# Kernel optimization log

Measured on AMD Instinct MI355X. Metric: run time of the kernel, lower is better.

## Reference

```python
import jax, jax.numpy as jnp
import numpy as np

GROUP = 64  # group_size from module


def setup_inputs() -> dict:
    key = jax.random.key(0)
    ks = jax.random.split(key, 7)
    B, S, N, K = 4, 2048, 4096, 4096  # in_features=N, out_features=K
    G = N // GROUP
    x = jax.random.normal(ks[0], (B, S, N), dtype=jnp.float32)
    W_q = jax.random.randint(ks[1], (K, N), 0, 16, dtype=jnp.int32)  # 4-bit codes
    scales = jax.random.uniform(ks[2], (K, G), dtype=jnp.float32, minval=0.01, maxval=1.0)
    zeros = jax.random.uniform(ks[3], (K, G), dtype=jnp.float32, minval=0.0, maxval=15.0)
    mask = jax.random.randint(ks[4], (K, N), 0, 2, dtype=jnp.int32)  # unstructured sparsity mask
    scale2 = jax.random.uniform(ks[5], (K, 1), dtype=jnp.float32, minval=0.5, maxval=1.5)
    bias = jax.random.normal(ks[6], (K,), dtype=jnp.float32)
    return {"x": x, "W_q": W_q, "scales": scales, "zeros": zeros,
            "mask": mask, "scale2": scale2, "bias": bias}


def _dequantize_sparse_sinq(W_q, scales, zeros, mask, scale2, dtype):
    # W_q: (K, N) int codes; scales/zeros: (K, N//GROUP) per-(row,group);
    # scale2: (K, 1) second (Sinkhorn) row scale; mask: (K, N) sparsity mask.
    K, N = W_q.shape
    G = N // GROUP
    Wg = W_q.astype(dtype).reshape(K, G, GROUP)
    W = (Wg - zeros[:, :, None]) * scales[:, :, None]  # grouped affine dequant
    W = W.reshape(K, N) * scale2                       # dual-scale compensation
    W = W * mask.astype(dtype)                         # apply unstructured sparsity
    return W


def reference(x, W_q, scales, zeros, mask, scale2, bias):
    W = _dequantize_sparse_sinq(W_q, scales, zeros, mask, scale2, x.dtype)  # (K, N)
    out = jnp.einsum('bsn,kn->bsk', x, W) + bias  # x @ W.T + bias
    return out
```

## Files before the change

kernel.cpp:

```cpp
#include <hip/hip_runtime.h>


#define M_DIM 8192
#define N_DIM 4096
#define K_DIM 4096
#define BK 32
#define NT (N_DIM / BK)

typedef __bf16 bf16;
typedef __attribute__((ext_vector_type(8))) bf16 bf16x8;
typedef __attribute__((ext_vector_type(4))) float f32x4;

__global__ __launch_bounds__(256) void cvt_x_kernel(const float* __restrict__ x,
                                                    bf16* __restrict__ xb) {
  const long total = (long)M_DIM * N_DIM / 8;
  const long stride = (long)gridDim.x * blockDim.x;
  for (long t = (long)blockIdx.x * blockDim.x + threadIdx.x; t < total; t += stride) {
    const long e = t * 8;
    const float4 v0 = *reinterpret_cast<const float4*>(x + e);
    const float4 v1 = *reinterpret_cast<const float4*>(x + e + 4);
    bf16x8 o;
    o[0] = (bf16)v0.x; o[1] = (bf16)v0.y; o[2] = (bf16)v0.z; o[3] = (bf16)v0.w;
    o[4] = (bf16)v1.x; o[5] = (bf16)v1.y; o[6] = (bf16)v1.z; o[7] = (bf16)v1.w;
    *reinterpret_cast<bf16x8*>(xb + e) = o;
  }
}

__global__ __launch_bounds__(256) void deq_w_kernel(const int* __restrict__ Wq,
                                                    const float* __restrict__ scales,
                                                    const float* __restrict__ zeros,
                                                    const int* __restrict__ mask,
                                                    const float* __restrict__ scale2,
                                                    bf16* __restrict__ wb) {
  const int total = K_DIM * (N_DIM / 8);
  const int stride = gridDim.x * blockDim.x;
  for (int t = blockIdx.x * blockDim.x + threadIdx.x; t < total; t += stride) {
    const int k = t >> 9;
    const int n0 = (t & 511) << 3;
    const int g = n0 >> 6;
    const float s = scales[(k << 6) + g] * scale2[k];
    const float z = zeros[(k << 6) + g];
    const long base = (long)k * N_DIM + n0;
    const int4 q0 = *reinterpret_cast<const int4*>(Wq + base);
    const int4 q1 = *reinterpret_cast<const int4*>(Wq + base + 4);
    const int4 m0 = *reinterpret_cast<const int4*>(mask + base);
    const int4 m1 = *reinterpret_cast<const int4*>(mask + base + 4);
    bf16x8 o;
    o[0] = (bf16)(((float)q0.x - z) * s * (float)m0.x);
    o[1] = (bf16)(((float)q0.y - z) * s * (float)m0.y);
    o[2] = (bf16)(((float)q0.z - z) * s * (float)m0.z);
    o[3] = (bf16)(((float)q0.w - z) * s * (float)m0.w);
    o[4] = (bf16)(((float)q1.x - z) * s * (float)m1.x);
    o[5] = (bf16)(((float)q1.y - z) * s * (float)m1.y);
    o[6] = (bf16)(((float)q1.z - z) * s * (float)m1.z);
    o[7] = (bf16)(((float)q1.w - z) * s * (float)m1.w);
    *reinterpret_cast<bf16x8*>(wb + base) = o;
  }
}

__device__ inline void gload16(const bf16* g, bf16* l) {
  __builtin_amdgcn_global_load_lds(
      (const __attribute__((address_space(1))) void*)g,
      (__attribute__((address_space(3))) void*)l, 16, 0, 0);
}

__global__ __launch_bounds__(512, 2) void gemm_kernel(const bf16* __restrict__ xb,
                                                      const bf16* __restrict__ wb,
                                                      const float* __restrict__ bias,
                                                      float* __restrict__ out) {
  __shared__ bf16 lds[65536];

  const int tid = threadIdx.x;
  const int lane = tid & 63;
  const int w = tid >> 6;
  const int wr = w >> 2;
  const int wc = w & 3;

  const int gid = blockIdx.x;
  const int swz = ((gid & 7) << 6) | (gid >> 3);
  const int bm = swz & 31;
  const int bk = swz >> 5;
  const long m0 = (long)bm * 256;
  const long k0 = (long)bk * 256;

  const bf16* srcA0; const bf16* srcA1; const bf16* srcB0; const bf16* srcB1;
  {
    const int p0 = w * 1024 + lane * 16;
    const int rp0 = p0 >> 7;
    const int v0 = ((p0 >> 4) & 7) ^ (rp0 & 7);
    const int row0 = rp0 * 2 + (v0 >> 2), col0 = (v0 & 3) * 8;
    const int p1 = 8192 + w * 1024 + lane * 16;
    const int rp1 = p1 >> 7;
    const int v1 = ((p1 >> 4) & 7) ^ (rp1 & 7);
    const int row1 = rp1 * 2 + (v1 >> 2), col1 = (v1 & 3) * 8;
    srcA0 = xb + (m0 + row0) * N_DIM + col0;
    srcA1 = xb + (m0 + row1) * N_DIM + col1;
    srcB0 = wb + (k0 + row0) * N_DIM + col0;
    srcB1 = wb + (k0 + row1) * N_DIM + col1;
  }

  const int halfrow = (lane & 15) >> 1;
  const int xsw = (((lane & 1) << 2) | (lane >> 4)) ^ halfrow;
  const int frBase = halfrow * 64 + xsw * 8;
  const int aOff = wr * 4096 + frBase;
  const int bOff = 8192 + wc * 2048 + frBase;

  auto STAGE = [&](int t) {
    bf16* base = lds + (t & 3) * 16384;
    const int ko = t * BK;
    gload16(srcA0 + ko, base + w * 512);
    gload16(srcA1 + ko, base + 4096 + w * 512);
    gload16(srcB0 + ko, base + 8192 + w * 512);
    gload16(srcB1 + ko, base + 12288 + w * 512);
  };

  f32x4 acc[8][4] = {};

  STAGE(0); STAGE(1); STAGE(2);
  asm volatile("s_waitcnt vmcnt(8)" ::: "memory");
  asm volatile("s_barrier" ::: "memory");

  for (int t = 0; t < NT; ++t) {
    const bf16* base = lds + (t & 3) * 16384;
    bf16x8 af[8], bfr[4];
#pragma unroll
    for (int mi = 0; mi < 8; ++mi)
      af[mi] = *reinterpret_cast<const bf16x8*>(base + aOff + mi * 512);
#pragma unroll
    for (int ni = 0; ni < 4; ++ni)
      bfr[ni] = *reinterpret_cast<const bf16x8*>(base + bOff + ni * 512);

    if (t + 3 < NT) STAGE(t + 3);

    if (t < NT - 3)       asm volatile("s_waitcnt vmcnt(8)" ::: "memory");
    else if (t == NT - 3) asm volatile("s_waitcnt vmcnt(4)" ::: "memory");
    else                  asm volatile("s_waitcnt vmcnt(0)" ::: "memory");
    asm volatile("s_waitcnt lgkmcnt(0)" ::: "memory");
    asm volatile("s_barrier" ::: "memory");
    __builtin_amdgcn_sched_barrier(0);

    __builtin_amdgcn_s_setprio(1);
#pragma unroll
    for (int mi = 0; mi < 8; ++mi)
#pragma unroll
      for (int ni = 0; ni < 4; ++ni)
        acc[mi][ni] = __builtin_amdgcn_mfma_f32_16x16x32_bf16(af[mi], bfr[ni],
                                                              acc[mi][ni], 0, 0, 0);
    __builtin_amdgcn_s_setprio(0);
  }

  const int ocol0 = (int)k0 + wc * 64 + (lane & 15);
  const int orow0 = (int)m0 + wr * 128 + (lane >> 4) * 4;
#pragma unroll
  for (int ni = 0; ni < 4; ++ni) {
    const float bv = bias[ocol0 + ni * 16];
#pragma unroll
    for (int mi = 0; mi < 8; ++mi)
#pragma unroll
      for (int r = 0; r < 4; ++r)
        out[(long)(orow0 + mi * 16 + r) * K_DIM + ocol0 + ni * 16] =
            acc[mi][ni][r] + bv;
  }
}

extern "C" void kernel_launch(void* const* d_in, const int* in_sizes, int n_in,
                              void* d_out, int out_size, void* d_ws, size_t ws_size,
                              hipStream_t stream) {
  const float* x      = (const float*)d_in[0];
  const int*   Wq     = (const int*)d_in[1];
  const float* scales = (const float*)d_in[2];
  const float* zeros  = (const float*)d_in[3];
  const int*   mask   = (const int*)d_in[4];
  const float* scale2 = (const float*)d_in[5];
  const float* bias   = (const float*)d_in[6];
  float* out = (float*)d_out;

  bf16* xb = (bf16*)d_ws;
  bf16* wb = (bf16*)((char*)d_ws + (size_t)M_DIM * N_DIM * 2);

  cvt_x_kernel<<<2048, 256, 0, stream>>>(x, xb);
  deq_w_kernel<<<2048, 256, 0, stream>>>(Wq, scales, zeros, mask, scale2, wb);

  gemm_kernel<<<512, 512, 0, stream>>>(xb, wb, bias, out);
}
```

Baseline: 321.3 us.

## Restructure GEMM main loop into ping-pong half-tile stages with interleaved loads

The GEMM main loop moves from a 4-deep ring of BK=32 stages to two 64-wide K buffers. Each 64-wide tile is split into four half-tile phases: LDS fragment reads and global-to-LDS staging of A or B halves are interleaved with 8x2 MFMA blocks, separated by barriers. The goal is to spread memory traffic across the compute and shrink fragment register pressure (the B fragments are split into halves). In exchange it adds many more barriers per K step and a shallower prefetch distance, and the waitcnt bookkeeping is intricate.

```diff
diff --git a/kernel.cpp b/kernel.cpp
--- a/kernel.cpp
+++ b/kernel.cpp
@@ -4,8 +4,7 @@
 #define M_DIM 8192
 #define N_DIM 4096
 #define K_DIM 4096
-#define BK 32
-#define NT (N_DIM / BK)
+#define NTILE 64
 
 typedef __bf16 bf16;
 typedef __attribute__((ext_vector_type(8))) bf16 bf16x8;
@@ -64,6 +63,12 @@
       (__attribute__((address_space(3))) void*)l, 16, 0, 0);
 }
 
+#define BARRIER asm volatile("s_barrier" ::: "memory")
+#define LGKM0   asm volatile("s_waitcnt lgkmcnt(0)" ::: "memory")
+#define VM4     asm volatile("s_waitcnt vmcnt(4)" ::: "memory")
+#define VM0     asm volatile("s_waitcnt vmcnt(0)" ::: "memory")
+#define SBAR    __builtin_amdgcn_sched_barrier(0)
+
 __global__ __launch_bounds__(512, 2) void gemm_kernel(const bf16* __restrict__ xb,
                                                       const bf16* __restrict__ wb,
                                                       const float* __restrict__ bias,
@@ -83,7 +88,7 @@
   const long m0 = (long)bm * 256;
   const long k0 = (long)bk * 256;
 
-  const bf16* srcA0; const bf16* srcA1; const bf16* srcB0; const bf16* srcB1;
+  const bf16 *srcA0, *srcA1, *srcB0, *srcB1;
   {
     const int p0 = w * 1024 + lane * 16;
     const int rp0 = p0 >> 7;
@@ -101,52 +106,92 @@
 
   const int halfrow = (lane & 15) >> 1;
   const int xsw = (((lane & 1) << 2) | (lane >> 4)) ^ halfrow;
-  const int frBase = halfrow * 64 + xsw * 8;
-  const int aOff = wr * 4096 + frBase;
-  const int bOff = 8192 + wc * 2048 + frBase;
-
-  auto STAGE = [&](int t) {
-    bf16* base = lds + (t & 3) * 16384;
-    const int ko = t * BK;
-    gload16(srcA0 + ko, base + w * 512);
-    gload16(srcA1 + ko, base + 4096 + w * 512);
-    gload16(srcB0 + ko, base + 8192 + w * 512);
-    gload16(srcB1 + ko, base + 12288 + w * 512);
-  };
+  const int aBase = wr * 4096 + halfrow * 64 + xsw * 8;
+  const int bBase = wc * 2048 + halfrow * 64 + xsw * 8;
 
   f32x4 acc[8][4] = {};
-
-  STAGE(0); STAGE(1); STAGE(2);
-  asm volatile("s_waitcnt vmcnt(8)" ::: "memory");
-  asm volatile("s_barrier" ::: "memory");
-
-  for (int t = 0; t < NT; ++t) {
-    const bf16* base = lds + (t & 3) * 16384;
-    bf16x8 af[8], bfr[4];
+  bf16x8 a[8], b01[2], b23[2];
+
+  auto LD_A = [&](int bufbase, int kk) {
 #pragma unroll
     for (int mi = 0; mi < 8; ++mi)
-      af[mi] = *reinterpret_cast<const bf16x8*>(base + aOff + mi * 512);
-#pragma unroll
-    for (int ni = 0; ni < 4; ++ni)
-      bfr[ni] = *reinterpret_cast<const bf16x8*>(base + bOff + ni * 512);
-
-    if (t + 3 < NT) STAGE(t + 3);
-
-    if (t < NT - 3)       asm volatile("s_waitcnt vmcnt(8)" ::: "memory");
-    else if (t == NT - 3) asm volatile("s_waitcnt vmcnt(4)" ::: "memory");
-    else                  asm volatile("s_waitcnt vmcnt(0)" ::: "memory");
-    asm volatile("s_waitcnt lgkmcnt(0)" ::: "memory");
-    asm volatile("s_barrier" ::: "memory");
-    __builtin_amdgcn_sched_barrier(0);
-
+      a[mi] = *reinterpret_cast<const bf16x8*>(lds + bufbase + kk * 8192 + aBase + mi * 512);
+  };
+  auto LD_B = [&](bf16x8* b, int bufbase, int kk, int nh) {
+#pragma unroll
+    for (int j = 0; j < 2; ++j)
+      b[j] = *reinterpret_cast<const bf16x8*>(lds + bufbase + 16384 + kk * 8192 + bBase + (nh * 2 + j) * 512);
+  };
+  auto MFMA8x2 = [&](bf16x8* b, int nh) {
     __builtin_amdgcn_s_setprio(1);
 #pragma unroll
     for (int mi = 0; mi < 8; ++mi)
 #pragma unroll
-      for (int ni = 0; ni < 4; ++ni)
-        acc[mi][ni] = __builtin_amdgcn_mfma_f32_16x16x32_bf16(af[mi], bfr[ni],
-                                                              acc[mi][ni], 0, 0, 0);
+      for (int j = 0; j < 2; ++j)
+        acc[mi][nh * 2 + j] = __builtin_amdgcn_mfma_f32_16x16x32_bf16(
+            a[mi], b[j], acc[mi][nh * 2 + j], 0, 0, 0);
     __builtin_amdgcn_s_setprio(0);
+  };
+  auto STAGE2 = [&](const bf16* s0, const bf16* s1, int dstoff) {
+    gload16(s0, lds + dstoff + w * 512);
+    gload16(s1, lds + dstoff + 4096 + w * 512);
+  };
+
+  STAGE2(srcA0, srcA1, 0);
+  STAGE2(srcB0, srcB1, 16384);
+  STAGE2(srcA0 + 32, srcA1 + 32, 8192);
+  STAGE2(srcB0 + 32, srcB1 + 32, 24576);
+  VM4;
+  BARRIER;
+
+  for (int tp = 0; tp < NTILE / 2; ++tp) {
+    const int koA = (2 * tp + 1) * 64;
+    const int koB = (2 * tp + 2) * 64;
+    const bool st = (tp < NTILE / 2 - 1);
+
+    LD_A(0, 0); LD_B(b01, 0, 0, 0);
+    STAGE2(srcA0 + koA, srcA1 + koA, 32768 + 0);
+    BARRIER; LGKM0; SBAR;
+    MFMA8x2(b01, 0); SBAR;
+    BARRIER;
+    LD_B(b23, 0, 0, 1);
+    STAGE2(srcB0 + koA, srcB1 + koA, 32768 + 16384);
+    VM4; BARRIER; LGKM0; SBAR;
+    MFMA8x2(b23, 1); SBAR;
+    BARRIER;
+    LD_A(0, 1); LD_B(b01, 0, 1, 0);
+    STAGE2(srcA0 + koA + 32, srcA1 + koA + 32, 32768 + 8192);
+    BARRIER; LGKM0; SBAR;
+    MFMA8x2(b01, 0); SBAR;
+    BARRIER;
+    LD_B(b23, 0, 1, 1);
+    STAGE2(srcB0 + koA + 32, srcB1 + koA + 32, 32768 + 24576);
+    VM4; BARRIER; LGKM0; SBAR;
+    MFMA8x2(b23, 1); SBAR;
+    BARRIER;
+
+    LD_A(32768, 0); LD_B(b01, 32768, 0, 0);
+    if (st) STAGE2(srcA0 + koB, srcA1 + koB, 0);
+    BARRIER; LGKM0; SBAR;
+    MFMA8x2(b01, 0); SBAR;
+    BARRIER;
+    LD_B(b23, 32768, 0, 1);
+    if (st) STAGE2(srcB0 + koB, srcB1 + koB, 16384);
+    if (st) { VM4; } else { VM0; }
+    BARRIER; LGKM0; SBAR;
+    MFMA8x2(b23, 1); SBAR;
+    BARRIER;
+    LD_A(32768, 1); LD_B(b01, 32768, 1, 0);
+    if (st) STAGE2(srcA0 + koB + 32, srcA1 + koB + 32, 8192);
+    BARRIER; LGKM0; SBAR;
+    MFMA8x2(b01, 0); SBAR;
+    BARRIER;
+    LD_B(b23, 32768, 1, 1);
+    if (st) STAGE2(srcB0 + koB + 32, srcB1 + koB + 32, 24576);
+    if (st) { VM4; } else { VM0; }
+    BARRIER; LGKM0; SBAR;
+    MFMA8x2(b23, 1); SBAR;
+    BARRIER;
   }
 
   const int ocol0 = (int)k0 + wc * 64 + (lane & 15);
```

After: 328.7 us. +2.3%, slower.

## Restructure GEMM mainloop into 64-wide K tiles with quadrant-interleaved loads and MFMAs

Applied to the files above, without the earlier changes.

Raises the K tile from 32 to 64 and replaces the 4-stage ring of small tiles with a double-buffered 64-wide tile. Each tile is split into four MFMA quadrants, with LDS fragment reads and global-to-LDS loads for later tiles issued between them. The aim is to hide global and LDS latency behind MFMA work and to cut barriers and waits per unit of compute. In exchange it adds more barriers inside each tile, and the prefetch/vmcnt bookkeeping is more complex and easier to get wrong.

```diff
diff --git a/kernel.cpp b/kernel.cpp
--- a/kernel.cpp
+++ b/kernel.cpp
@@ -4,8 +4,7 @@
 #define M_DIM 8192
 #define N_DIM 4096
 #define K_DIM 4096
-#define BK 32
-#define NT (N_DIM / BK)
+#define NT 64
 
 typedef __bf16 bf16;
 typedef __attribute__((ext_vector_type(8))) bf16 bf16x8;
@@ -64,6 +63,12 @@
       (__attribute__((address_space(3))) void*)l, 16, 0, 0);
 }
 
+#define BARRIER asm volatile("s_barrier" ::: "memory")
+#define LGKM0   asm volatile("s_waitcnt lgkmcnt(0)" ::: "memory")
+#define VM6     asm volatile("s_waitcnt vmcnt(6)" ::: "memory")
+#define VM0     asm volatile("s_waitcnt vmcnt(0)" ::: "memory")
+#define SBAR    __builtin_amdgcn_sched_barrier(0)
+
 __global__ __launch_bounds__(512, 2) void gemm_kernel(const bf16* __restrict__ xb,
                                                       const bf16* __restrict__ wb,
                                                       const float* __restrict__ bias,
@@ -83,73 +88,100 @@
   const long m0 = (long)bm * 256;
   const long k0 = (long)bk * 256;
 
-  const bf16* srcA0; const bf16* srcA1; const bf16* srcB0; const bf16* srcB1;
-  {
-    const int p0 = w * 1024 + lane * 16;
-    const int rp0 = p0 >> 7;
-    const int v0 = ((p0 >> 4) & 7) ^ (rp0 & 7);
-    const int row0 = rp0 * 2 + (v0 >> 2), col0 = (v0 & 3) * 8;
-    const int p1 = 8192 + w * 1024 + lane * 16;
-    const int rp1 = p1 >> 7;
-    const int v1 = ((p1 >> 4) & 7) ^ (rp1 & 7);
-    const int row1 = rp1 * 2 + (v1 >> 2), col1 = (v1 & 3) * 8;
-    srcA0 = xb + (m0 + row0) * N_DIM + col0;
-    srcA1 = xb + (m0 + row1) * N_DIM + col1;
-    srcB0 = wb + (k0 + row0) * N_DIM + col0;
-    srcB1 = wb + (k0 + row1) * N_DIM + col1;
-  }
-
-  const int halfrow = (lane & 15) >> 1;
-  const int xsw = (((lane & 1) << 2) | (lane >> 4)) ^ halfrow;
-  const int frBase = halfrow * 64 + xsw * 8;
-  const int aOff = wr * 4096 + frBase;
-  const int bOff = 8192 + wc * 2048 + frBase;
-
-  auto STAGE = [&](int t) {
-    bf16* base = lds + (t & 3) * 16384;
-    const int ko = t * BK;
-    gload16(srcA0 + ko, base + w * 512);
-    gload16(srcA1 + ko, base + 4096 + w * 512);
-    gload16(srcB0 + ko, base + 8192 + w * 512);
-    gload16(srcB1 + ko, base + 12288 + w * 512);
-  };
+  const int browA = tid >> 3;
+  const int slotA = (tid & 7) ^ (browA & 7);
+  const bf16* baseA = xb + (m0 + browA) * N_DIM + slotA * 8;
+  const int u = tid & 255;
+  const int wcb = tid >> 8;
+  const int browB = u >> 3;
+  const int slotB = (u & 7) ^ (browB & 7);
+  const bf16* baseB = wb + (k0 + wcb * 64 + browB) * N_DIM + slotB * 8;
+
+  const int ln15 = lane & 15;
+  const int x0 = (lane >> 4) ^ (lane & 7);
+  int aoffk[2], boffk[2];
+#pragma unroll
+  for (int kk = 0; kk < 2; ++kk) {
+    const int x = x0 ^ (kk << 2);
+    aoffk[kk] = (wr * 128 + ln15) * 64 + x * 8;
+    boffk[kk] = 16384 + (wc * 64 + ln15) * 64 + x * 8;
+  }
 
   f32x4 acc[8][4] = {};
-
-  STAGE(0); STAGE(1); STAGE(2);
-  asm volatile("s_waitcnt vmcnt(8)" ::: "memory");
-  asm volatile("s_barrier" ::: "memory");
-
-  for (int t = 0; t < NT; ++t) {
-    const bf16* base = lds + (t & 3) * 16384;
-    bf16x8 af[8], bfr[4];
-#pragma unroll
-    for (int mi = 0; mi < 8; ++mi)
-      af[mi] = *reinterpret_cast<const bf16x8*>(base + aOff + mi * 512);
-#pragma unroll
-    for (int ni = 0; ni < 4; ++ni)
-      bfr[ni] = *reinterpret_cast<const bf16x8*>(base + bOff + ni * 512);
-
-    if (t + 3 < NT) STAGE(t + 3);
-
-    if (t < NT - 3)       asm volatile("s_waitcnt vmcnt(8)" ::: "memory");
-    else if (t == NT - 3) asm volatile("s_waitcnt vmcnt(4)" ::: "memory");
-    else                  asm volatile("s_waitcnt vmcnt(0)" ::: "memory");
-    asm volatile("s_waitcnt lgkmcnt(0)" ::: "memory");
-    asm volatile("s_barrier" ::: "memory");
-    __builtin_amdgcn_sched_barrier(0);
-
+  bf16x8 af[4][2], bfA[2][2], bfB[2][2];
+
+  auto STA = [&](int tt, int bsel, int h) {
+    const bf16* s = baseA + (long)(h * 64) * N_DIM + tt * 64;
+    bf16* d = lds + bsel * 32768 + h * 4096 + (tid << 3);
+    gload16(s, d);
+    gload16(s + (long)128 * N_DIM, d + 8192);
+  };
+  auto STB = [&](int tt, int bsel, int h) {
+    const bf16* s = baseB + (long)(h * 32) * N_DIM + tt * 64;
+    bf16* d = lds + bsel * 32768 + 16384 + wcb * 4096 + h * 2048 + (u << 3);
+    gload16(s, d);
+    gload16(s + (long)128 * N_DIM, d + 8192);
+  };
+  auto LDA = [&](int cb, int mh) {
+#pragma unroll
+    for (int mf = 0; mf < 4; ++mf)
+#pragma unroll
+      for (int kk = 0; kk < 2; ++kk)
+        af[mf][kk] = *reinterpret_cast<const bf16x8*>(
+            lds + cb + aoffk[kk] + mh * 4096 + mf * 1024);
+  };
+  auto LDB = [&](bf16x8 (*bf)[2], int cb, int nh) {
+#pragma unroll
+    for (int nf = 0; nf < 2; ++nf)
+#pragma unroll
+      for (int kk = 0; kk < 2; ++kk)
+        bf[nf][kk] = *reinterpret_cast<const bf16x8*>(
+            lds + cb + boffk[kk] + nh * 2048 + nf * 1024);
+  };
+  auto MFMA_Q = [&](bf16x8 (*bf)[2], int mh, int nh) {
     __builtin_amdgcn_s_setprio(1);
 #pragma unroll
-    for (int mi = 0; mi < 8; ++mi)
-#pragma unroll
-      for (int ni = 0; ni < 4; ++ni)
-        acc[mi][ni] = __builtin_amdgcn_mfma_f32_16x16x32_bf16(af[mi], bfr[ni],
-                                                              acc[mi][ni], 0, 0, 0);
+    for (int kk = 0; kk < 2; ++kk)
+#pragma unroll
+      for (int mf = 0; mf < 4; ++mf)
+#pragma unroll
+        for (int nf = 0; nf < 2; ++nf)
+          acc[mh * 4 + mf][nh * 2 + nf] = __builtin_amdgcn_mfma_f32_16x16x32_bf16(
+              af[mf][kk], bf[nf][kk], acc[mh * 4 + mf][nh * 2 + nf], 0, 0, 0);
     __builtin_amdgcn_s_setprio(0);
-  }
-
-  const int ocol0 = (int)k0 + wc * 64 + (lane & 15);
+  };
+
+  STA(0, 0, 0); STB(0, 0, 0); STB(0, 0, 1); STA(0, 0, 1);
+  STA(1, 1, 0); STB(1, 1, 0); STB(1, 1, 1);
+  VM6; BARRIER;
+
+  auto TILE = [&](int t, int c) {
+    const int cb = c * 32768;
+    LDA(cb, 0); LDB(bfA, cb, 0);
+    if (t + 1 < NT) STA(t + 1, c ^ 1, 1);
+    asm volatile("s_waitcnt lgkmcnt(8)" ::: "memory");
+    BARRIER; LGKM0; SBAR;
+    MFMA_Q(bfA, 0, 0); SBAR; BARRIER;
+    LDB(bfB, cb, 1);
+    if (t + 2 < NT) STA(t + 2, c, 0);
+    BARRIER; LGKM0; SBAR;
+    MFMA_Q(bfB, 0, 1); SBAR; BARRIER;
+    LDA(cb, 1);
+    if (t + 2 < NT) STB(t + 2, c, 0);
+    BARRIER; LGKM0; SBAR;
+    MFMA_Q(bfA, 1, 0); SBAR; BARRIER;
+    if (t + 2 < NT) STB(t + 2, c, 1);
+    if (t < NT - 2) { VM6; } else { VM0; }
+    BARRIER; LGKM0; SBAR;
+    MFMA_Q(bfB, 1, 1); SBAR; BARRIER;
+  };
+
+  for (int tp = 0; tp < NT / 2; ++tp) {
+    TILE(2 * tp, 0);
+    TILE(2 * tp + 1, 1);
+  }
+
+  const int ocol0 = (int)k0 + wc * 64 + ln15;
   const int orow0 = (int)m0 + wr * 128 + (lane >> 4) * 4;
 #pragma unroll
   for (int ni = 0; ni < 4; ++ni) {
```

Measured after the change: 303.1 us. 5.7% less time.
